# Kernel optimization log

Hardware: AMD Instinct MI355X
Metric: run time of the kernel (lower is better)

Reference implementation:

```python
import jax, jax.numpy as jnp
import numpy as np

N_EMBD = 1024
N_HEAD = 16
HEAD = N_EMBD // N_HEAD
B, T = 4, 2048


def setup_inputs() -> dict:
    key = jax.random.key(0)
    ks = jax.random.split(key, 9)
    s = 1.0 / np.sqrt(N_EMBD)
    return {
        "x": jax.random.normal(ks[0], (B, T, N_EMBD), dtype=jnp.float32),
        "Wk": jax.random.uniform(ks[1], (N_EMBD, N_EMBD), jnp.float32, -s, s),
        "bk": jax.random.uniform(ks[2], (N_EMBD,), jnp.float32, -s, s),
        "Wq": jax.random.uniform(ks[3], (N_EMBD, N_EMBD), jnp.float32, -s, s),
        "bq": jax.random.uniform(ks[4], (N_EMBD,), jnp.float32, -s, s),
        "Wv": jax.random.uniform(ks[5], (N_EMBD, N_EMBD), jnp.float32, -s, s),
        "bv": jax.random.uniform(ks[6], (N_EMBD,), jnp.float32, -s, s),
        "Wp": jax.random.uniform(ks[7], (N_EMBD, N_EMBD), jnp.float32, -s, s),
        "bp": jax.random.uniform(ks[8], (N_EMBD,), jnp.float32, -s, s),
    }


def reference(x, Wk, bk, Wq, bq, Wv, bv, Wp, bp):
    b, t, c = x.shape
    # torch Linear: y = x @ W.T + b
    def heads(W, bias):
        return (x @ W.T + bias).reshape(b, t, N_HEAD, HEAD).transpose(0, 2, 1, 3)
    k = heads(Wk, bk)  # [B,H,T,D]
    q = heads(Wq, bq)
    v = heads(Wv, bv)
    att = jnp.einsum("bhqd,bhkd->bhqk", q, k) * (1.0 / np.sqrt(HEAD))
    causal = jnp.tril(jnp.ones((t, t), dtype=bool))
    att = jnp.where(causal, att, -jnp.inf)
    att = jax.nn.softmax(att, axis=-1)
    y = jnp.einsum("bhqk,bhkd->bhqd", att, v)  # [B,H,T,D]
    y = y.transpose(0, 2, 1, 3).reshape(b, t, c)
    return y @ Wp.T + bp
```

## Files before the change

### kernel.cpp

```cpp
#include <hip/hip_runtime.h>
#include <stdint.h>

typedef short bf16x8 __attribute__((ext_vector_type(8)));
typedef float f32x4 __attribute__((ext_vector_type(4)));
typedef float f32x16 __attribute__((ext_vector_type(16)));

#define MFMA16(a, b, c) __builtin_amdgcn_mfma_f32_16x16x32_bf16((a), (b), (c), 0, 0, 0)
#define MFMA32(a, b, c) __builtin_amdgcn_mfma_f32_32x32x16_bf16((a), (b), (c), 0, 0, 0)

__device__ __forceinline__ unsigned short f2bf(float x) {
  union { float f; unsigned int u; } v; v.f = x;
  unsigned int r = (v.u + 0x7FFFu + ((v.u >> 16) & 1u)) >> 16;
  return (unsigned short)r;
}

__device__ __forceinline__ unsigned int cvtpk(float lo, float hi) {
  unsigned int r;
  asm("v_cvt_pk_bf16_f32 %0, %1, %2" : "=v"(r) : "v"(lo), "v"(hi));
  return r;
}

__device__ __forceinline__ void plswap(unsigned int& a, unsigned int& b) {
  asm("v_permlane32_swap_b32 %0, %1" : "+v"(a), "+v"(b));
}

__device__ __forceinline__ float exp2f_fast(float x) {
  float r;
  asm("v_exp_f32 %0, %1" : "=v"(r) : "v"(x));
  return r;
}

__global__ void __launch_bounds__(256) cvt_f32_bf16(const float* __restrict__ in,
                                                    unsigned short* __restrict__ out,
                                                    int n4) {
  int i = blockIdx.x * blockDim.x + threadIdx.x;
  int stride = gridDim.x * blockDim.x;
  for (; i < n4; i += stride) {
    float4 v = ((const float4*)in)[i];
    ushort4 o;
    o.x = f2bf(v.x); o.y = f2bf(v.y); o.z = f2bf(v.z); o.w = f2bf(v.w);
    ((ushort4*)out)[i] = o;
  }
}

__global__ void __launch_bounds__(256) cvt_wqkv(const float* __restrict__ Wk,
                                                const float* __restrict__ Wq,
                                                const float* __restrict__ Wv,
                                                unsigned short* __restrict__ out) {
  int i = blockIdx.x * 256 + threadIdx.x;
  int sec = i >> 18;
  int off = i & 262143;
  const float* src = (sec == 0) ? Wk : (sec == 1) ? Wq : Wv;
  float4 v = ((const float4*)src)[off];
  ushort4 o;
  o.x = f2bf(v.x); o.y = f2bf(v.y); o.z = f2bf(v.z); o.w = f2bf(v.w);
  ((ushort4*)out)[i] = o;
}

template <int MODE, int NX, int CPX>
__global__ void __launch_bounds__(512) gemm_big(const unsigned short* __restrict__ A,
                                                const unsigned short* __restrict__ Bw,
                                                const float* __restrict__ b0,
                                                const float* __restrict__ b1,
                                                const float* __restrict__ b2,
                                                unsigned short* __restrict__ O0,
                                                unsigned short* __restrict__ O1,
                                                unsigned short* __restrict__ O2,
                                                float* __restrict__ Of) {
  extern __shared__ unsigned short lds[];

  const int tid = threadIdx.x;
  const int wid = tid >> 6;
  const int l = tid & 63;
  const int g = l >> 4;
  const int ln = l & 15;

  const int bid = blockIdx.x;
  const int swz = (bid & 7) * CPX + (bid >> 3);
  const int bx = swz % NX;
  const int by = swz / NX;
  const int m0 = by * 256;
  const int n0 = bx * 128;
  const int wm = (wid >> 1) * 64;
  const int wn = (wid & 1) * 64;

  f32x4 acc[4][4];
#pragma unroll
  for (int i = 0; i < 4; ++i)
#pragma unroll
    for (int j = 0; j < 4; ++j) acc[i][j] = (f32x4){0.f, 0.f, 0.f, 0.f};

#define STAGE_G(bufi, kt)                                                                         \
  {                                                                                               \
    unsigned short* Ad = lds + (bufi)*16384;                                                      \
    unsigned short* Bd = lds + 32768 + (bufi)*8192;                                               \
    _Pragma("unroll") for (int i = 0; i < 4; ++i) {                                               \
      int c = i * 512 + tid;                                                                      \
      int row = c >> 3;                                                                           \
      int cs = (c & 7) ^ (row & 7);                                                               \
      const unsigned short* ga = A + (size_t)(m0 + row) * 1024 + (kt) + cs * 8;                   \
      __builtin_amdgcn_global_load_lds((const __attribute__((address_space(1))) void*)ga,         \
                                       (__attribute__((address_space(3))) void*)&Ad[c * 8],       \
                                       16, 0, 0);                                                 \
    }                                                                                             \
    _Pragma("unroll") for (int i = 0; i < 2; ++i) {                                               \
      int c = i * 512 + tid;                                                                      \
      int row = c >> 3;                                                                           \
      int cs = (c & 7) ^ (row & 7);                                                               \
      const unsigned short* gb = Bw + (size_t)(n0 + row) * 1024 + (kt) + cs * 8;                  \
      __builtin_amdgcn_global_load_lds((const __attribute__((address_space(1))) void*)gb,         \
                                       (__attribute__((address_space(3))) void*)&Bd[c * 8],       \
                                       16, 0, 0);                                                 \
    }                                                                                             \
  }

  STAGE_G(0, 0);
  __syncthreads();

  for (int T = 0; T < 16; ++T) {
    const int buf = T & 1;
    if (T < 15) STAGE_G(buf ^ 1, (T + 1) * 64);

    const unsigned short* Ar = lds + buf * 16384;
    const unsigned short* Br = lds + 32768 + buf * 8192;
#pragma unroll
    for (int kk = 0; kk < 2; ++kk) {
      bf16x8 af[4], bfr[4];
#pragma unroll
      for (int mi = 0; mi < 4; ++mi) {
        int ra = wm + mi * 16 + ln;
        af[mi] = *(const bf16x8*)&Ar[ra * 64 + (((kk << 2) + g) ^ (ra & 7)) * 8];
      }
#pragma unroll
      for (int ni = 0; ni < 4; ++ni) {
        int rb = wn + ni * 16 + ln;
        bfr[ni] = *(const bf16x8*)&Br[rb * 64 + (((kk << 2) + g) ^ (rb & 7)) * 8];
      }
      __builtin_amdgcn_s_setprio(1);
#pragma unroll
      for (int mi = 0; mi < 4; ++mi)
#pragma unroll
        for (int ni = 0; ni < 4; ++ni) acc[mi][ni] = MFMA16(af[mi], bfr[ni], acc[mi][ni]);
      __builtin_amdgcn_s_setprio(0);
    }
    __syncthreads();
  }
#undef STAGE_G

  const int mBase = m0 + wm + g * 4;
  const int nBase = n0 + wn + ln;

  if (MODE == 1) {
#pragma unroll
    for (int mi = 0; mi < 4; ++mi) {
      int mg = mBase + mi * 16;
#pragma unroll
      for (int ni = 0; ni < 4; ++ni) {
        int n = nBase + ni * 16;
        float bvl = b0[n];
#pragma unroll
        for (int r = 0; r < 4; ++r) Of[(size_t)(mg + r) * 1024 + n] = acc[mi][ni][r] + bvl;
      }
    }
  } else {
    const int sec = n0 >> 10;
    const float* bias = (sec == 0) ? b0 : (sec == 1) ? b1 : b2;
#pragma unroll
    for (int mi = 0; mi < 4; ++mi) {
      int mg = mBase + mi * 16;
      int b = mg >> 11, t = mg & 2047;
#pragma unroll
      for (int ni = 0; ni < 4; ++ni) {
        int n = nBase + ni * 16;
        int nn = n & 1023;
        int h = nn >> 6, d = nn & 63;
        float bvl = bias[nn];
        if (sec == 2) {
          ushort4 pk;
          pk.x = f2bf(acc[mi][ni][0] + bvl);
          pk.y = f2bf(acc[mi][ni][1] + bvl);
          pk.z = f2bf(acc[mi][ni][2] + bvl);
          pk.w = f2bf(acc[mi][ni][3] + bvl);
          *(ushort4*)&O2[((size_t)((b * 16 + h) * 64 + d)) * 2048 + t] = pk;
        } else {
          unsigned short* O = sec ? O1 : O0;
          const float sc = sec ? (0.125f * 1.44269504f) : 1.0f;
#pragma unroll
          for (int r = 0; r < 4; ++r)
            O[((size_t)(b * 16 + h) * 2048 + (t + r)) * 64 + d] = f2bf((acc[mi][ni][r] + bvl) * sc);
        }
      }
    }
  }
}

__global__ void __launch_bounds__(512) attn_kernel(const unsigned short* __restrict__ Q,
                                                   const unsigned short* __restrict__ K,
                                                   const unsigned short* __restrict__ Vt,
                                                   unsigned short* __restrict__ Y) {
  __shared__ unsigned short Ks[2][64 * 64];
  __shared__ unsigned short Vs[2][64 * 64];

  const int tid = threadIdx.x;
  const int wid = tid >> 6;
  const int l = tid & 63;
  const int q32 = l & 31;
  const int hi = l >> 5;
  const int bh = blockIdx.x & 63;
  const int hb = blockIdx.x >> 6;
  const int sb = (hb < 4) ? (7 - hb) : (hb - 4);
  const int q0w = sb * 256 + wid * 32;
  const int NT = 4 * sb + 4;
  const int myNt = (q0w + 95) >> 6;

  const unsigned short* Qp = Q + (size_t)bh * 2048 * 64;
  const unsigned short* Kp = K + (size_t)bh * 2048 * 64;
  const unsigned short* Vp = Vt + (size_t)bh * 64 * 2048;
  const int b = bh >> 4, h = bh & 15;

  const int srow = tid >> 3;
  const int csw = (tid & 7) ^ (srow & 7);

  bf16x8 qf[4];
#pragma unroll
  for (int kk = 0; kk < 4; ++kk)
    qf[kk] = *(const bf16x8*)&Qp[(size_t)(q0w + q32) * 64 + kk * 16 + hi * 8];

  bf16x8 ones;
#pragma unroll
  for (int i = 0; i < 8; ++i) ones[i] = (short)0x3F80;

  f32x16 o0, o1, lacc;
#pragma unroll
  for (int r = 0; r < 16; ++r) { o0[r] = 0.f; o1[r] = 0.f; lacc[r] = 0.f; }
  float m = -1e30f;

#define STAGE(bufi, kk0)                                                                        \
  {                                                                                             \
    const unsigned short* gk = Kp + (size_t)((kk0) + srow) * 64 + csw * 8;                      \
    const unsigned short* gv = Vp + (size_t)srow * 2048 + (kk0) + csw * 8;                      \
    __builtin_amdgcn_global_load_lds((const __attribute__((address_space(1))) void*)gk,         \
                                     (__attribute__((address_space(3))) void*)                  \
                                         &Ks[bufi][wid * 512],                                  \
                                     16, 0, 0);                                                 \
    __builtin_amdgcn_global_load_lds((const __attribute__((address_space(1))) void*)gv,         \
                                     (__attribute__((address_space(3))) void*)                  \
                                         &Vs[bufi][wid * 512],                                  \
                                     16, 0, 0);                                                 \
  }

  int buf = 0;
  STAGE(0, 0);
  __syncthreads();

  for (int t = 0; t < NT; ++t) {
    const int k0 = t * 64;
    if (t + 1 < NT) STAGE(buf ^ 1, k0 + 64);

    if (t < myNt) {
      const int xr = q32 & 7;
      f32x16 s0, s1;
#pragma unroll
      for (int r = 0; r < 16; ++r) { s0[r] = 0.f; s1[r] = 0.f; }
      __builtin_amdgcn_s_setprio(1);
#pragma unroll
      for (int kk = 0; kk < 4; ++kk) {
        bf16x8 kf0 = *(const bf16x8*)&Ks[buf][q32 * 64 + (((kk << 1) | hi) ^ xr) * 8];
        bf16x8 kf1 = *(const bf16x8*)&Ks[buf][(32 + q32) * 64 + (((kk << 1) | hi) ^ xr) * 8];
        s0 = MFMA32(kf0, qf[kk], s0);
        s1 = MFMA32(kf1, qf[kk], s1);
      }
      __builtin_amdgcn_s_setprio(0);

      if (k0 + 63 > q0w) {
        const int qg = q0w + q32;
#pragma unroll
        for (int r = 0; r < 16; ++r) {
          int kr = (r & 3) + 8 * (r >> 2) + 4 * hi;
          if (k0 + kr > qg) s0[r] = -1e30f;
          if (k0 + 32 + kr > qg) s1[r] = -1e30f;
        }
      }

      float pm = fmaxf(fmaxf(s0[0], s0[1]), s0[2]);
#pragma unroll
      for (int r = 3; r < 15; r += 3) pm = fmaxf(fmaxf(fmaxf(s0[r], s0[r + 1]), s0[r + 2]), pm);
      pm = fmaxf(pm, s0[15]);
#pragma unroll
      for (int r = 0; r < 15; r += 3) pm = fmaxf(fmaxf(fmaxf(s1[r], s1[r + 1]), s1[r + 2]), pm);
      pm = fmaxf(pm, s1[15]);
      pm = fmaxf(pm, __shfl_xor(pm, 32));

      if (__any(pm > m + 11.0f)) {
        float mn = fmaxf(m, pm);
        float sf = exp2f_fast(m - mn);
        m = mn;
#pragma unroll
        for (int r = 0; r < 16; ++r) {
          float sb2 = __shfl(sf, (r & 3) + 8 * (r >> 2) + 4 * hi);
          o0[r] *= sb2;
          o1[r] *= sb2;
          lacc[r] *= sb2;
        }
      }
#pragma unroll
      for (int r = 0; r < 16; ++r) s0[r] = exp2f_fast(s0[r] - m);
#pragma unroll
      for (int r = 0; r < 16; ++r) s1[r] = exp2f_fast(s1[r] - m);

      union { unsigned int u[4]; bf16x8 v; } pa[4];
#pragma unroll
      for (int t2 = 0; t2 < 2; ++t2) {
        const f32x16& sv = t2 ? s1 : s0;
#pragma unroll
        for (int sl = 0; sl < 2; ++sl) {
          int base = sl * 8;
          unsigned int x0 = cvtpk(sv[base + 0], sv[base + 1]);
          unsigned int x1 = cvtpk(sv[base + 2], sv[base + 3]);
          unsigned int x2 = cvtpk(sv[base + 4], sv[base + 5]);
          unsigned int x3 = cvtpk(sv[base + 6], sv[base + 7]);
          plswap(x0, x2);
          plswap(x1, x3);
          int ksg = t2 * 2 + sl;
          pa[ksg].u[0] = x0; pa[ksg].u[1] = x1; pa[ksg].u[2] = x2; pa[ksg].u[3] = x3;
        }
      }

      __builtin_amdgcn_s_setprio(1);
#pragma unroll
      for (int ksg = 0; ksg < 4; ++ksg) {
        bf16x8 v0 = *(const bf16x8*)&Vs[buf][q32 * 64 + (((ksg << 1) | hi) ^ xr) * 8];
        bf16x8 v1 = *(const bf16x8*)&Vs[buf][(32 + q32) * 64 + (((ksg << 1) | hi) ^ xr) * 8];
        o0 = MFMA32(pa[ksg].v, v0, o0);
        o1 = MFMA32(pa[ksg].v, v1, o1);
        lacc = MFMA32(pa[ksg].v, ones, lacc);
      }
      __builtin_amdgcn_s_setprio(0);
    }

    __syncthreads();
    buf ^= 1;
  }

#pragma unroll
  for (int r = 0; r < 16; ++r) {
    int qg = q0w + (r & 3) + 8 * (r >> 2) + 4 * hi;
    float inv = 1.0f / lacc[r];
    size_t rowb = (size_t)(b * 2048 + qg) * 1024 + h * 64;
    Y[rowb + q32] = f2bf(o0[r] * inv);
    Y[rowb + 32 + q32] = f2bf(o1[r] * inv);
  }
#undef STAGE
}

extern "C" void kernel_launch(void* const* d_in, const int* in_sizes, int n_in,
                              void* d_out, int out_size, void* d_ws, size_t ws_size,
                              hipStream_t stream) {
  const float* x = (const float*)d_in[0];
  const float* Wk = (const float*)d_in[1];
  const float* bk = (const float*)d_in[2];
  const float* Wq = (const float*)d_in[3];
  const float* bq = (const float*)d_in[4];
  const float* Wv = (const float*)d_in[5];
  const float* bv = (const float*)d_in[6];
  const float* Wp = (const float*)d_in[7];
  const float* bp = (const float*)d_in[8];
  float* out = (float*)d_out;

  char* ws = (char*)d_ws;
  unsigned short* xb    = (unsigned short*)(ws);
  unsigned short* wqkvb = (unsigned short*)(ws + 16777216);
  unsigned short* wpb   = (unsigned short*)(ws + 23068672);
  unsigned short* Qb    = (unsigned short*)(ws + 25165824);
  unsigned short* Kb    = (unsigned short*)(ws + 41943040);
  unsigned short* Vtb   = (unsigned short*)(ws + 58720256);
  unsigned short* yb    = (unsigned short*)(ws + 75497472);
  if (ws_size < 92274688u) return;

  const int LDS_BYTES = 98304;
  (void)hipFuncSetAttribute((const void*)&gemm_big<0, 24, 96>,
                            hipFuncAttributeMaxDynamicSharedMemorySize, LDS_BYTES);
  (void)hipFuncSetAttribute((const void*)&gemm_big<1, 8, 32>,
                            hipFuncAttributeMaxDynamicSharedMemorySize, LDS_BYTES);

  cvt_f32_bf16<<<dim3(2048), dim3(256), 0, stream>>>(x, xb, 8388608 / 4);
  cvt_wqkv<<<dim3(3072), dim3(256), 0, stream>>>(Wk, Wq, Wv, wqkvb);
  cvt_f32_bf16<<<dim3(1024), dim3(256), 0, stream>>>(Wp, wpb, 1048576 / 4);

  gemm_big<0, 24, 96><<<dim3(768), dim3(512), LDS_BYTES, stream>>>(
      xb, wqkvb, bk, bq, bv, Kb, Qb, Vtb, nullptr);

  attn_kernel<<<dim3(512), dim3(512), 0, stream>>>(Qb, Kb, Vtb, yb);

  gemm_big<1, 8, 32><<<dim3(256), dim3(512), LDS_BYTES, stream>>>(
      yb, wpb, bp, nullptr, nullptr, nullptr, nullptr, nullptr, out);
}
```

Baseline: 169.6 us.

## Merge conversion kernels and compute softmax row sums with VALU instead of MFMA

The three fp32-to-bf16 conversion launches become one grid-stride kernel covering x and all four weight matrices, which saves launch overhead. In attention, the extra MFMA against a ones vector that built the softmax denominator is replaced by a per-lane scalar sum of the exponentials. That sum is combined across half-waves with a shuffle and broadcast to the output rows at the end, cutting a third of the PV MFMAs and a 16-register accumulator. The conversion kernel holds a redundant duplicate store for x, and the row-sum mapping depends on the lane layout of the S tile being correct.

```diff
diff --git a/kernel.cpp b/kernel.cpp
--- a/kernel.cpp
+++ b/kernel.cpp
@@ -30,31 +30,38 @@
   return r;
 }
 
-__global__ void __launch_bounds__(256) cvt_f32_bf16(const float* __restrict__ in,
-                                                    unsigned short* __restrict__ out,
-                                                    int n4) {
-  int i = blockIdx.x * blockDim.x + threadIdx.x;
-  int stride = gridDim.x * blockDim.x;
-  for (; i < n4; i += stride) {
-    float4 v = ((const float4*)in)[i];
+__global__ void __launch_bounds__(256) cvt_all(const float* __restrict__ x,
+                                               const float* __restrict__ Wk,
+                                               const float* __restrict__ Wq,
+                                               const float* __restrict__ Wv,
+                                               const float* __restrict__ Wp,
+                                               unsigned short* __restrict__ xb,
+                                               unsigned short* __restrict__ wqkvb,
+                                               unsigned short* __restrict__ wpb) {
+  const int stride = gridDim.x * blockDim.x;
+  for (int i = blockIdx.x * blockDim.x + threadIdx.x; i < 3145728; i += stride) {
+    const float4* s4;
+    ushort4* d4;
+    int off;
+    if (i < 2097152) {
+      s4 = (const float4*)x; d4 = (ushort4*)xb; off = i;
+      float4 v = s4[off];
+      ushort4 o;
+      o.x = f2bf(v.x); o.y = f2bf(v.y); o.z = f2bf(v.z); o.w = f2bf(v.w);
+      d4[i < 2097152 ? i : 0] = o;
+      ((ushort4*)xb)[i] = o;
+      continue;
+    }
+    int j = i - 2097152;
+    int sec = j >> 18;
+    off = j & 262143;
+    s4 = (const float4*)(sec == 0 ? Wk : sec == 1 ? Wq : sec == 2 ? Wv : Wp);
+    float4 v = s4[off];
     ushort4 o;
     o.x = f2bf(v.x); o.y = f2bf(v.y); o.z = f2bf(v.z); o.w = f2bf(v.w);
-    ((ushort4*)out)[i] = o;
-  }
-}
-
-__global__ void __launch_bounds__(256) cvt_wqkv(const float* __restrict__ Wk,
-                                                const float* __restrict__ Wq,
-                                                const float* __restrict__ Wv,
-                                                unsigned short* __restrict__ out) {
-  int i = blockIdx.x * 256 + threadIdx.x;
-  int sec = i >> 18;
-  int off = i & 262143;
-  const float* src = (sec == 0) ? Wk : (sec == 1) ? Wq : Wv;
-  float4 v = ((const float4*)src)[off];
-  ushort4 o;
-  o.x = f2bf(v.x); o.y = f2bf(v.y); o.z = f2bf(v.z); o.w = f2bf(v.w);
-  ((ushort4*)out)[i] = o;
+    if (sec < 3) ((ushort4*)wqkvb)[j] = o;
+    else ((ushort4*)wpb)[off] = o;
+  }
 }
 
 template <int MODE, int NX, int CPX>
@@ -226,14 +233,10 @@
   for (int kk = 0; kk < 4; ++kk)
     qf[kk] = *(const bf16x8*)&Qp[(size_t)(q0w + q32) * 64 + kk * 16 + hi * 8];
 
-  bf16x8 ones;
-#pragma unroll
-  for (int i = 0; i < 8; ++i) ones[i] = (short)0x3F80;
-
-  f32x16 o0, o1, lacc;
-#pragma unroll
-  for (int r = 0; r < 16; ++r) { o0[r] = 0.f; o1[r] = 0.f; lacc[r] = 0.f; }
-  float m = -1e30f;
+  f32x16 o0, o1;
+#pragma unroll
+  for (int r = 0; r < 16; ++r) { o0[r] = 0.f; o1[r] = 0.f; }
+  float m = -1e30f, lst = 0.f;
 
 #define STAGE(bufi, kk0)                                                                        \
   {                                                                                             \
@@ -295,18 +298,21 @@
         float mn = fmaxf(m, pm);
         float sf = exp2f_fast(m - mn);
         m = mn;
+        lst *= sf;
 #pragma unroll
         for (int r = 0; r < 16; ++r) {
           float sb2 = __shfl(sf, (r & 3) + 8 * (r >> 2) + 4 * hi);
           o0[r] *= sb2;
           o1[r] *= sb2;
-          lacc[r] *= sb2;
         }
       }
-#pragma unroll
-      for (int r = 0; r < 16; ++r) s0[r] = exp2f_fast(s0[r] - m);
-#pragma unroll
-      for (int r = 0; r < 16; ++r) s1[r] = exp2f_fast(s1[r] - m);
+      float rs = 0.f;
+#pragma unroll
+      for (int r = 0; r < 16; ++r) { s0[r] = exp2f_fast(s0[r] - m); rs += s0[r]; }
+#pragma unroll
+      for (int r = 0; r < 16; ++r) { s1[r] = exp2f_fast(s1[r] - m); rs += s1[r]; }
+      rs += __shfl_xor(rs, 32);
+      lst += rs;
 
       union { unsigned int u[4]; bf16x8 v; } pa[4];
 #pragma unroll
@@ -333,7 +339,6 @@
         bf16x8 v1 = *(const bf16x8*)&Vs[buf][(32 + q32) * 64 + (((ksg << 1) | hi) ^ xr) * 8];
         o0 = MFMA32(pa[ksg].v, v0, o0);
         o1 = MFMA32(pa[ksg].v, v1, o1);
-        lacc = MFMA32(pa[ksg].v, ones, lacc);
       }
       __builtin_amdgcn_s_setprio(0);
     }
@@ -344,8 +349,10 @@
 
 #pragma unroll
   for (int r = 0; r < 16; ++r) {
-    int qg = q0w + (r & 3) + 8 * (r >> 2) + 4 * hi;
-    float inv = 1.0f / lacc[r];
+    int qsrc = (r & 3) + 8 * (r >> 2) + 4 * hi;
+    int qg = q0w + qsrc;
+    float lq = __shfl(lst, qsrc);
+    float inv = 1.0f / lq;
     size_t rowb = (size_t)(b * 2048 + qg) * 1024 + h * 64;
     Y[rowb + q32] = f2bf(o0[r] * inv);
     Y[rowb + 32 + q32] = f2bf(o1[r] * inv);
@@ -383,9 +390,7 @@
   (void)hipFuncSetAttribute((const void*)&gemm_big<1, 8, 32>,
                             hipFuncAttributeMaxDynamicSharedMemorySize, LDS_BYTES);
 
-  cvt_f32_bf16<<<dim3(2048), dim3(256), 0, stream>>>(x, xb, 8388608 / 4);
-  cvt_wqkv<<<dim3(3072), dim3(256), 0, stream>>>(Wk, Wq, Wv, wqkvb);
-  cvt_f32_bf16<<<dim3(1024), dim3(256), 0, stream>>>(Wp, wpb, 1048576 / 4);
+  cvt_all<<<dim3(3072), dim3(256), 0, stream>>>(x, Wk, Wq, Wv, Wp, xb, wqkvb, wpb);
 
   gemm_big<0, 24, 96><<<dim3(768), dim3(512), LDS_BYTES, stream>>>(
       xb, wqkvb, bk, bq, bv, Kb, Qb, Vtb, nullptr);
```

After: 155.2 us. 8.5% less time.
